# Performance work log

Measured on AMD Instinct MI355X. Metric: run time of the kernel, lower is better.

## Reference

```python
import jax, jax.numpy as jnp
import numpy as np

H, D, G = 8, 32, 32          # heads, dim_head, slice_num
SCALE = D ** -0.5
EPS_LN = 1e-5
EPS_NORM = 1e-5


def layer_norm(x, g, b):
    mu = x.mean(-1, keepdims=True)
    var = x.var(-1, keepdims=True)
    return (x - mu) / jnp.sqrt(var + EPS_LN) * g + b


def setup_inputs() -> dict:
    key = jax.random.key(0)
    ks = jax.random.split(key, 12)
    B, N, C = 4, 32768, 256

    def rn(k, shape, s=0.02):
        return jax.random.normal(k, shape, dtype=jnp.float32) * s

    return {
        "fx": jax.random.normal(ks[0], (B, N, C), dtype=jnp.float32),
        "ln_g": jnp.ones((C,), jnp.float32), "ln_b": jnp.zeros((C,), jnp.float32),
        "Wx": rn(ks[1], (C, H * D)), "bx": jnp.zeros((H * D,), jnp.float32),
        "Wfx": rn(ks[2], (C, H * D)), "bfx": jnp.zeros((H * D,), jnp.float32),
        "Ws": rn(ks[3], (D, G), 0.1), "bs": jnp.zeros((G,), jnp.float32),
        "temp": jnp.full((1, H, 1, 1), 0.5, jnp.float32),
        "Wq": rn(ks[4], (D, D)), "Wk": rn(ks[5], (D, D)), "Wv": rn(ks[6], (D, D)),
        "tln_g": jnp.ones((D,), jnp.float32), "tln_b": jnp.zeros((D,), jnp.float32),
        "W1": rn(ks[7], (D, 4 * D)), "b1": jnp.zeros((4 * D,), jnp.float32),
        "W2": rn(ks[8], (4 * D, D)), "b2": jnp.zeros((D,), jnp.float32),
        "Wo": rn(ks[9], (H * D, C)), "bo": jnp.zeros((C,), jnp.float32),
    }


def reference(fx, ln_g, ln_b, Wx, bx, Wfx, bfx, Ws, bs, temp,
              Wq, Wk, Wv, tln_g, tln_b, W1, b1, W2, b2, Wo, bo):
    B, N, C = fx.shape
    fx_norm = layer_norm(fx, ln_g, ln_b)

    # soft-slice dispatch: project points to per-head features [B,H,N,D]
    x_mid = (fx_norm @ Wx + bx).reshape(B, N, H, D).transpose(0, 2, 1, 3)
    fx_mid = (fx_norm @ Wfx + bfx).reshape(B, N, H, D).transpose(0, 2, 1, 3)
    slice_w = jax.nn.softmax((x_mid @ Ws + bs) / temp, axis=-1)      # [B,H,N,G]
    slice_norm = slice_w.sum(axis=2)                                  # [B,H,G]
    slice_token = jnp.einsum('bhnd,bhng->bhgd', fx_mid, slice_w)
    slice_token = slice_token / (slice_norm + EPS_NORM)[..., None]    # [B,H,G,D]

    # small attention over G=32 slice tokens
    q = slice_token @ Wq
    k = slice_token @ Wk
    v = slice_token @ Wv
    attn = jax.nn.softmax(jnp.einsum('bhgd,bhkd->bhgk', q, k) * SCALE, axis=-1)
    out_tok = jnp.einsum('bhgk,bhkd->bhgd', attn, v) + slice_token

    # token MLP (LN -> Linear -> GELU -> Linear) with residual
    h = layer_norm(out_tok, tln_g, tln_b)
    tokens = (jax.nn.gelu(h @ W1 + b1, approximate=False) @ W2 + b2) + out_tok

    # weighted combine back to points, output projection, residual
    out_x = jnp.einsum('bhgd,bhng->bhnd', tokens, slice_w)
    out_x = out_x.transpose(0, 2, 1, 3).reshape(B, N, H * D)
    return out_x @ Wo + bo + fx_norm
```

## Files before the change

kernel.cpp:

```cpp
#include <hip/hip_runtime.h>
#include <hip/hip_bf16.h>
#include <math.h>

static const int kN = 32768;

typedef __attribute__((ext_vector_type(8))) short short8;
typedef __attribute__((ext_vector_type(4))) float f32x4;

__device__ inline unsigned short f2bf(float x) {
    union { float f; unsigned u; } v; v.f = x;
    unsigned r = v.u + 0x7FFF + ((v.u >> 16) & 1);
    return (unsigned short)(r >> 16);
}

__global__ void k_zero(float* __restrict__ p, int n)
{
    int i = blockIdx.x * 256 + threadIdx.x;
    if (i < n) p[i] = 0.f;
}

__global__ void k_prep(const float* __restrict__ Wx, const float* __restrict__ Ws,
                       const float* __restrict__ bx, const float* __restrict__ bs,
                       const float* __restrict__ Wfx,
                       unsigned short* __restrict__ WxsT, unsigned short* __restrict__ WfxT,
                       float* __restrict__ blog)
{
    __shared__ float ws_s[1024];
    int tid = threadIdx.x;
    for (int i = tid; i < 1024; i += 256) ws_s[i] = Ws[i];
    __syncthreads();
    int c = blockIdx.x;
    int h = tid >> 5, g = tid & 31;
    const float* wrow = &Wx[c * 256 + h * 32];
    float s = 0.f;
    #pragma unroll
    for (int d = 0; d < 32; d++) s += wrow[d] * ws_s[d * 32 + g];
    WxsT[tid * 256 + c] = f2bf(s);
    WfxT[tid * 256 + c] = f2bf(Wfx[c * 256 + tid]);
    if (c == 0) {
        float t = 0.f;
        #pragma unroll
        for (int d = 0; d < 32; d++) t += bx[h * 32 + d] * ws_s[d * 32 + g];
        blog[tid] = t + bs[g];
    }
}

__global__ __launch_bounds__(256) void k_ln(const float* __restrict__ fx,
                                            const float* __restrict__ gam,
                                            const float* __restrict__ bet,
                                            float* __restrict__ out,
                                            unsigned short* __restrict__ outb)
{
    int lane = threadIdx.x & 63;
    long row = (long)blockIdx.x * 4 + (threadIdx.x >> 6);
    float4 v = *(const float4*)&fx[row * 256 + lane * 4];
    float s  = v.x + v.y + v.z + v.w;
    float ss = v.x * v.x + v.y * v.y + v.z * v.z + v.w * v.w;
    for (int off = 32; off; off >>= 1) { s += __shfl_down(s, off); ss += __shfl_down(ss, off); }
    s = __shfl(s, 0); ss = __shfl(ss, 0);
    float mu = s * (1.f / 256.f);
    float rstd = rsqrtf(ss * (1.f / 256.f) - mu * mu + 1e-5f);
    float4 gv = *(const float4*)&gam[lane * 4];
    float4 bv = *(const float4*)&bet[lane * 4];
    float4 o;
    o.x = (v.x - mu) * rstd * gv.x + bv.x;
    o.y = (v.y - mu) * rstd * gv.y + bv.y;
    o.z = (v.z - mu) * rstd * gv.z + bv.z;
    o.w = (v.w - mu) * rstd * gv.w + bv.w;
    *(float4*)&out[row * 256 + lane * 4] = o;
    ushort4 ob;
    ob.x = f2bf(o.x); ob.y = f2bf(o.y); ob.z = f2bf(o.z); ob.w = f2bf(o.w);
    *(ushort4*)&outb[row * 256 + lane * 4] = ob;
}

__global__ __launch_bounds__(256) void k_gemm_mid_mfma(
    const unsigned short* __restrict__ Abf,
    const unsigned short* __restrict__ WxsT, const unsigned short* __restrict__ WfxT,
    const float* __restrict__ blog, const float* __restrict__ bfx,
    const float* __restrict__ temp,
    unsigned short* __restrict__ swb, unsigned short* __restrict__ fmb)
{
    const int mode = blockIdx.y;
    const unsigned short* __restrict__ WT = mode ? WfxT : WxsT;
    const int tid = threadIdx.x;
    const int w = tid >> 6, l = tid & 63;
    const int r16 = l & 15, g4 = l >> 4;
    const long row0 = (long)blockIdx.x * 64;

    __shared__ unsigned short sA[64][40];
    __shared__ unsigned short sB[256][40];

    f32x4 acc[4][4];
    #pragma unroll
    for (int mf = 0; mf < 4; mf++)
        #pragma unroll
        for (int nf = 0; nf < 4; nf++) acc[mf][nf] = (f32x4){0.f, 0.f, 0.f, 0.f};

    const int arow = tid >> 2, apart = tid & 3;
    for (int k0 = 0; k0 < 256; k0 += 32) {
        *(uint4*)&sA[arow][apart * 8] =
            *(const uint4*)&Abf[(row0 + arow) * 256 + k0 + apart * 8];
        #pragma unroll
        for (int p = 0; p < 4; p++) {
            int col = p * 64 + arow;
            *(uint4*)&sB[col][apart * 8] = *(const uint4*)&WT[col * 256 + k0 + apart * 8];
        }
        __syncthreads();
        short8 af[4], bfr[4];
        #pragma unroll
        for (int mf = 0; mf < 4; mf++) af[mf] = *(const short8*)&sA[mf * 16 + r16][g4 * 8];
        #pragma unroll
        for (int nf = 0; nf < 4; nf++) bfr[nf] = *(const short8*)&sB[w * 64 + nf * 16 + r16][g4 * 8];
        #pragma unroll
        for (int mf = 0; mf < 4; mf++)
            #pragma unroll
            for (int nf = 0; nf < 4; nf++)
                acc[mf][nf] = __builtin_amdgcn_mfma_f32_16x16x32_bf16(
                    af[mf], bfr[nf], acc[mf][nf], 0, 0, 0);
        __syncthreads();
    }

    if (mode == 0) {
        float rt0 = 1.0f / temp[w * 2], rt1 = 1.0f / temp[w * 2 + 1];
        float bl00 = blog[w * 64 + r16],      bl01 = blog[w * 64 + 16 + r16];
        float bl10 = blog[w * 64 + 32 + r16], bl11 = blog[w * 64 + 48 + r16];
        #pragma unroll
        for (int mf = 0; mf < 4; mf++) {
            #pragma unroll
            for (int ri = 0; ri < 4; ri++) {
                long row = row0 + mf * 16 + g4 * 4 + ri;
                {
                    float z0 = (acc[mf][0][ri] + bl00) * rt0;
                    float z1 = (acc[mf][1][ri] + bl01) * rt0;
                    float m = fmaxf(z0, z1);
                    m = fmaxf(m, __shfl_xor(m, 1)); m = fmaxf(m, __shfl_xor(m, 2));
                    m = fmaxf(m, __shfl_xor(m, 4)); m = fmaxf(m, __shfl_xor(m, 8));
                    float e0 = __expf(z0 - m), e1 = __expf(z1 - m);
                    float sum = e0 + e1;
                    sum += __shfl_xor(sum, 1); sum += __shfl_xor(sum, 2);
                    sum += __shfl_xor(sum, 4); sum += __shfl_xor(sum, 8);
                    float inv = 1.0f / sum;
                    swb[row * 256 + w * 64 + r16]      = f2bf(e0 * inv);
                    swb[row * 256 + w * 64 + 16 + r16] = f2bf(e1 * inv);
                }
                {
                    float z0 = (acc[mf][2][ri] + bl10) * rt1;
                    float z1 = (acc[mf][3][ri] + bl11) * rt1;
                    float m = fmaxf(z0, z1);
                    m = fmaxf(m, __shfl_xor(m, 1)); m = fmaxf(m, __shfl_xor(m, 2));
                    m = fmaxf(m, __shfl_xor(m, 4)); m = fmaxf(m, __shfl_xor(m, 8));
                    float e0 = __expf(z0 - m), e1 = __expf(z1 - m);
                    float sum = e0 + e1;
                    sum += __shfl_xor(sum, 1); sum += __shfl_xor(sum, 2);
                    sum += __shfl_xor(sum, 4); sum += __shfl_xor(sum, 8);
                    float inv = 1.0f / sum;
                    swb[row * 256 + w * 64 + 32 + r16] = f2bf(e0 * inv);
                    swb[row * 256 + w * 64 + 48 + r16] = f2bf(e1 * inv);
                }
            }
        }
    } else {
        float bb[4];
        #pragma unroll
        for (int nf = 0; nf < 4; nf++) bb[nf] = bfx[w * 64 + nf * 16 + r16];
        #pragma unroll
        for (int mf = 0; mf < 4; mf++)
            #pragma unroll
            for (int nf = 0; nf < 4; nf++)
                #pragma unroll
                for (int ri = 0; ri < 4; ri++) {
                    long row = row0 + mf * 16 + g4 * 4 + ri;
                    fmb[row * 256 + w * 64 + nf * 16 + r16] = f2bf(acc[mf][nf][ri] + bb[nf]);
                }
    }
}

__global__ __launch_bounds__(256) void k_reduce(
    const unsigned short* __restrict__ swb, const unsigned short* __restrict__ fmb,
    float* __restrict__ tok_acc, float* __restrict__ nrm_acc)
{
    const int bh = blockIdx.y;
    const int b = bh >> 3, h = bh & 7;
    const int tid = threadIdx.x;
    const int g = tid >> 3, dq = tid & 7, d0 = dq * 4;
    __shared__ float sw_t[64][36];
    __shared__ float fm_t[64][36];
    float4 acc = make_float4(0.f, 0.f, 0.f, 0.f);
    float nacc = 0.f;
    long base = (long)b * kN + (long)blockIdx.x * 2048;
    const int r = tid >> 2, q = tid & 3;

    for (int t0 = 0; t0 < 2048; t0 += 64) {
        long ga = (base + t0 + r) * 256 + h * 32 + q * 8;
        uint4 wv = *(const uint4*)&swb[ga];
        uint4 fv = *(const uint4*)&fmb[ga];
        __syncthreads();
        const unsigned* wu = (const unsigned*)&wv;
        const unsigned* fu = (const unsigned*)&fv;
        #pragma unroll
        for (int e = 0; e < 4; e++) {
            union { unsigned u; float f; } lo, hi;
            lo.u = wu[e] << 16; hi.u = wu[e] & 0xFFFF0000u;
            sw_t[r][q * 8 + 2 * e] = lo.f; sw_t[r][q * 8 + 2 * e + 1] = hi.f;
            lo.u = fu[e] << 16; hi.u = fu[e] & 0xFFFF0000u;
            fm_t[r][q * 8 + 2 * e] = lo.f; fm_t[r][q * 8 + 2 * e + 1] = hi.f;
        }
        __syncthreads();
        #pragma unroll 4
        for (int rr = 0; rr < 64; rr++) {
            float wgt = sw_t[rr][g];
            float4 f = *(const float4*)&fm_t[rr][d0];
            acc.x += wgt * f.x; acc.y += wgt * f.y; acc.z += wgt * f.z; acc.w += wgt * f.w;
            if (dq == 0) nacc += wgt;
        }
    }
    float* ta = &tok_acc[(bh * 32 + g) * 32 + d0];
    atomicAdd(&ta[0], acc.x); atomicAdd(&ta[1], acc.y);
    atomicAdd(&ta[2], acc.z); atomicAdd(&ta[3], acc.w);
    if (dq == 0) atomicAdd(&nrm_acc[bh * 32 + g], nacc);
}

__global__ __launch_bounds__(256) void k_tokens(
    const float* __restrict__ tok_acc, const float* __restrict__ nrm_acc,
    const float* __restrict__ Wq, const float* __restrict__ Wk, const float* __restrict__ Wv,
    const float* __restrict__ tlng, const float* __restrict__ tlnb,
    const float* __restrict__ W1, const float* __restrict__ b1,
    const float* __restrict__ W2, const float* __restrict__ b2,
    const float* __restrict__ Wo, unsigned short* __restrict__ tokWoT)
{
    const int bh = blockIdx.x, b = bh >> 3, h = bh & 7;
    const int tid = threadIdx.x;
    const int g = tid >> 3, dq = tid & 7, d0 = dq * 4;
    __shared__ float t[32][32], qm[32][32], km[32][32], vm[32][32];
    __shared__ float att[32][33], ot[32][32], hn[32][32], tk[32][32];
    __shared__ float h1[32][128];
    __shared__ float mu_s[32], rs_s[32];

    {
        float inv = 1.0f / (nrm_acc[bh * 32 + g] + 1e-5f);
        #pragma unroll
        for (int u = 0; u < 4; u++)
            t[g][d0 + u] = tok_acc[(bh * 32 + g) * 32 + d0 + u] * inv;
    }
    __syncthreads();
    #pragma unroll
    for (int u = 0; u < 4; u++) {
        int d = d0 + u;
        float sq = 0.f, sk = 0.f, sv = 0.f;
        for (int dd = 0; dd < 32; dd++) {
            float tv = t[g][dd];
            sq = fmaf(tv, Wq[dd * 32 + d], sq);
            sk = fmaf(tv, Wk[dd * 32 + d], sk);
            sv = fmaf(tv, Wv[dd * 32 + d], sv);
        }
        qm[g][d] = sq; km[g][d] = sk; vm[g][d] = sv;
    }
    __syncthreads();
    const float SC = 0.17677669529663687f;
    #pragma unroll
    for (int u = 0; u < 4; u++) {
        int gk = d0 + u;
        float s = 0.f;
        for (int dd = 0; dd < 32; dd++) s = fmaf(qm[g][dd], km[gk][dd], s);
        att[g][gk] = s * SC;
    }
    __syncthreads();
    if (tid < 32) {
        float m = -1e30f;
        for (int j = 0; j < 32; j++) m = fmaxf(m, att[tid][j]);
        float s = 0.f;
        for (int j = 0; j < 32; j++) { float e = expf(att[tid][j] - m); att[tid][j] = e; s += e; }
        float inv = 1.0f / s;
        for (int j = 0; j < 32; j++) att[tid][j] *= inv;
    }
    __syncthreads();
    #pragma unroll
    for (int u = 0; u < 4; u++) {
        int d = d0 + u;
        float s = 0.f;
        for (int kk = 0; kk < 32; kk++) s = fmaf(att[g][kk], vm[kk][d], s);
        ot[g][d] = s + t[g][d];
    }
    __syncthreads();
    if (tid < 32) {
        float s = 0.f, ss = 0.f;
        for (int dd = 0; dd < 32; dd++) { float v = ot[tid][dd]; s += v; ss += v * v; }
        float mu = s * (1.f / 32.f);
        mu_s[tid] = mu;
        rs_s[tid] = rsqrtf(ss * (1.f / 32.f) - mu * mu + 1e-5f);
    }
    __syncthreads();
    #pragma unroll
    for (int u = 0; u < 4; u++) {
        int d = d0 + u;
        hn[g][d] = (ot[g][d] - mu_s[g]) * rs_s[g] * tlng[d] + tlnb[d];
    }
    __syncthreads();
    for (int c = dq * 16; c < dq * 16 + 16; c++) {
        float s = b1[c];
        for (int dd = 0; dd < 32; dd++) s = fmaf(hn[g][dd], W1[dd * 128 + c], s);
        h1[g][c] = 0.5f * s * (1.0f + erff(s * 0.70710678118654752f));
    }
    __syncthreads();
    #pragma unroll
    for (int u = 0; u < 4; u++) {
        int d = d0 + u;
        float s = b2[d];
        for (int c = 0; c < 128; c++) s = fmaf(h1[g][c], W2[c * 32 + d], s);
        tk[g][d] = s + ot[g][d];
    }
    __syncthreads();
    {
        int c0 = dq * 32;
        for (int c = c0; c < c0 + 32; c++) {
            float s = 0.f;
            for (int dd = 0; dd < 32; dd++) s = fmaf(tk[g][dd], Wo[(h * 32 + dd) * 256 + c], s);
            tokWoT[(size_t)b * 65536 + c * 256 + h * 32 + g] = f2bf(s);
        }
    }
}

__global__ __launch_bounds__(256) void k_gemm_out_mfma(
    const unsigned short* __restrict__ Abf,
    const unsigned short* __restrict__ tokWoT,
    const float* __restrict__ bo, const float* __restrict__ fx_norm,
    float* __restrict__ out)
{
    const int tid = threadIdx.x;
    const int w = tid >> 6, l = tid & 63;
    const int r16 = l & 15, g4 = l >> 4;
    const long row0 = (long)blockIdx.x * 64;
    const int b = (int)(row0 >> 15);
    const unsigned short* __restrict__ WT = tokWoT + (size_t)b * 65536;

    __shared__ unsigned short sA[64][40];
    __shared__ unsigned short sB[256][40];

    f32x4 acc[4][4];
    #pragma unroll
    for (int mf = 0; mf < 4; mf++)
        #pragma unroll
        for (int nf = 0; nf < 4; nf++) acc[mf][nf] = (f32x4){0.f, 0.f, 0.f, 0.f};

    const int arow = tid >> 2, apart = tid & 3;
    for (int k0 = 0; k0 < 256; k0 += 32) {
        *(uint4*)&sA[arow][apart * 8] =
            *(const uint4*)&Abf[(row0 + arow) * 256 + k0 + apart * 8];
        #pragma unroll
        for (int p = 0; p < 4; p++) {
            int col = p * 64 + arow;
            *(uint4*)&sB[col][apart * 8] = *(const uint4*)&WT[col * 256 + k0 + apart * 8];
        }
        __syncthreads();
        short8 af[4], bfr[4];
        #pragma unroll
        for (int mf = 0; mf < 4; mf++) af[mf] = *(const short8*)&sA[mf * 16 + r16][g4 * 8];
        #pragma unroll
        for (int nf = 0; nf < 4; nf++) bfr[nf] = *(const short8*)&sB[w * 64 + nf * 16 + r16][g4 * 8];
        #pragma unroll
        for (int mf = 0; mf < 4; mf++)
            #pragma unroll
            for (int nf = 0; nf < 4; nf++)
                acc[mf][nf] = __builtin_amdgcn_mfma_f32_16x16x32_bf16(
                    af[mf], bfr[nf], acc[mf][nf], 0, 0, 0);
        __syncthreads();
    }

    float bb[4];
    #pragma unroll
    for (int nf = 0; nf < 4; nf++) bb[nf] = bo[w * 64 + nf * 16 + r16];
    #pragma unroll
    for (int mf = 0; mf < 4; mf++)
        #pragma unroll
        for (int nf = 0; nf < 4; nf++)
            #pragma unroll
            for (int ri = 0; ri < 4; ri++) {
                long row = row0 + mf * 16 + g4 * 4 + ri;
                int col = w * 64 + nf * 16 + r16;
                out[row * 256 + col] = acc[mf][nf][ri] + bb[nf] + fx_norm[row * 256 + col];
            }
}

extern "C" void kernel_launch(void* const* d_in, const int* in_sizes, int n_in,
                              void* d_out, int out_size, void* d_ws, size_t ws_size,
                              hipStream_t stream)
{
    const float* fx   = (const float*)d_in[0];
    const float* ln_g = (const float*)d_in[1];
    const float* ln_b = (const float*)d_in[2];
    const float* Wx   = (const float*)d_in[3];
    const float* bx   = (const float*)d_in[4];
    const float* Wfx  = (const float*)d_in[5];
    const float* bfx  = (const float*)d_in[6];
    const float* Ws   = (const float*)d_in[7];
    const float* bs   = (const float*)d_in[8];
    const float* temp = (const float*)d_in[9];
    const float* Wq   = (const float*)d_in[10];
    const float* Wk   = (const float*)d_in[11];
    const float* Wv   = (const float*)d_in[12];
    const float* tlng = (const float*)d_in[13];
    const float* tlnb = (const float*)d_in[14];
    const float* W1   = (const float*)d_in[15];
    const float* b1   = (const float*)d_in[16];
    const float* W2   = (const float*)d_in[17];
    const float* b2   = (const float*)d_in[18];
    const float* Wo   = (const float*)d_in[19];
    const float* bo   = (const float*)d_in[20];
    float* out = (float*)d_out;

    char* ws = (char*)d_ws;
    float*          fx_norm = (float*)(ws + 0);
    unsigned short* fxn_bf  = (unsigned short*)(ws + 134217728);
    unsigned short* swb     = (unsigned short*)(ws + 201326592);
    unsigned short* fmb     = (unsigned short*)(ws + 268435456);
    unsigned short* WxsT    = (unsigned short*)(ws + 335544320);
    unsigned short* WfxT    = (unsigned short*)(ws + 335675392);
    float*          blog    = (float*)(ws + 335806464);
    float*          tok_acc = (float*)(ws + 335807488);
    float*          nrm_acc = (float*)(ws + 335938560);
    unsigned short* tokWoT  = (unsigned short*)(ws + 335942656);
    if (ws_size < 336466944ULL) return;

    k_prep<<<256, 256, 0, stream>>>(Wx, Ws, bx, bs, Wfx, WxsT, WfxT, blog);
    k_ln<<<32768, 256, 0, stream>>>(fx, ln_g, ln_b, fx_norm, fxn_bf);
    k_gemm_mid_mfma<<<dim3(2048, 2), 256, 0, stream>>>(fxn_bf, WxsT, WfxT, blog, bfx, temp,
                                                       swb, fmb);
    k_zero<<<132, 256, 0, stream>>>(tok_acc, 33792);
    k_reduce<<<dim3(16, 32), 256, 0, stream>>>(swb, fmb, tok_acc, nrm_acc);
    k_tokens<<<32, 256, 0, stream>>>(tok_acc, nrm_acc, Wq, Wk, Wv, tlng, tlnb,
                                     W1, b1, W2, b2, Wo, tokWoT);
    k_gemm_out_mfma<<<2048, 256, 0, stream>>>(swb, tokWoT, bo, fx_norm, out);
}
```

Baseline: 685.9 us.

## Restructure projection GEMMs with register-resident weights and LDS-staged coalesced stores

Result: slower. 706.8 us (+3.0%).

```diff
diff --git a/kernel.cpp b/kernel.cpp
--- a/kernel.cpp
+++ b/kernel.cpp
@@ -6,6 +6,13 @@
 
 typedef __attribute__((ext_vector_type(8))) short short8;
 typedef __attribute__((ext_vector_type(4))) float f32x4;
+
+typedef __attribute__((address_space(1))) const void* gas_t;
+typedef __attribute__((address_space(3))) void* las_t;
+
+__device__ __forceinline__ void gload16(const void* g, void* l) {
+    __builtin_amdgcn_global_load_lds((gas_t)g, (las_t)l, 16, 0, 0);
+}
 
 __device__ inline unsigned short f2bf(float x) {
     union { float f; unsigned u; } v; v.f = x;
@@ -73,105 +80,135 @@
     *(ushort4*)&outb[row * 256 + lane * 4] = ob;
 }
 
-__global__ __launch_bounds__(256) void k_gemm_mid_mfma(
+__global__ __launch_bounds__(512, 2) void k_gemm_mid_v3(
     const unsigned short* __restrict__ Abf,
     const unsigned short* __restrict__ WxsT, const unsigned short* __restrict__ WfxT,
     const float* __restrict__ blog, const float* __restrict__ bfx,
     const float* __restrict__ temp,
     unsigned short* __restrict__ swb, unsigned short* __restrict__ fmb)
 {
-    const int mode = blockIdx.y;
-    const unsigned short* __restrict__ WT = mode ? WfxT : WxsT;
     const int tid = threadIdx.x;
     const int w = tid >> 6, l = tid & 63;
     const int r16 = l & 15, g4 = l >> 4;
-    const long row0 = (long)blockIdx.x * 64;
-
-    __shared__ unsigned short sA[64][40];
-    __shared__ unsigned short sB[256][40];
-
-    f32x4 acc[4][4];
-    #pragma unroll
-    for (int mf = 0; mf < 4; mf++)
-        #pragma unroll
-        for (int nf = 0; nf < 4; nf++) acc[mf][nf] = (f32x4){0.f, 0.f, 0.f, 0.f};
-
-    const int arow = tid >> 2, apart = tid & 3;
-    for (int k0 = 0; k0 < 256; k0 += 32) {
-        *(uint4*)&sA[arow][apart * 8] =
-            *(const uint4*)&Abf[(row0 + arow) * 256 + k0 + apart * 8];
-        #pragma unroll
-        for (int p = 0; p < 4; p++) {
-            int col = p * 64 + arow;
-            *(uint4*)&sB[col][apart * 8] = *(const uint4*)&WT[col * 256 + k0 + apart * 8];
-        }
-        __syncthreads();
-        short8 af[4], bfr[4];
-        #pragma unroll
-        for (int mf = 0; mf < 4; mf++) af[mf] = *(const short8*)&sA[mf * 16 + r16][g4 * 8];
-        #pragma unroll
-        for (int nf = 0; nf < 4; nf++) bfr[nf] = *(const short8*)&sB[w * 64 + nf * 16 + r16][g4 * 8];
+    const int blk = blockIdx.x;
+
+    __shared__ unsigned short sA[2][64][32];
+    __shared__ unsigned short etile[64][264];
+
+    const unsigned short* WT = (w < 4) ? (WxsT + (size_t)(w * 64) * 256)
+                                       : (WfxT + (size_t)((w - 4) * 64) * 256);
+    short8 bq[4][8];
+    #pragma unroll
+    for (int nf = 0; nf < 4; nf++)
+        #pragma unroll
+        for (int ks = 0; ks < 8; ks++)
+            bq[nf][ks] = *(const short8*)&WT[(size_t)(nf * 16 + r16) * 256 + ks * 32 + g4 * 8];
+
+    float rt0 = 0.f, rt1 = 0.f, bl0 = 0.f, bl1 = 0.f, bl2 = 0.f, bl3 = 0.f;
+    float bf0 = 0.f, bf1 = 0.f, bf2 = 0.f, bf3 = 0.f;
+    if (w < 4) {
+        rt0 = 1.0f / temp[w * 2]; rt1 = 1.0f / temp[w * 2 + 1];
+        bl0 = blog[w * 64 + r16];      bl1 = blog[w * 64 + 16 + r16];
+        bl2 = blog[w * 64 + 32 + r16]; bl3 = blog[w * 64 + 48 + r16];
+    } else {
+        bf0 = bfx[(w - 4) * 64 + r16];      bf1 = bfx[(w - 4) * 64 + 16 + r16];
+        bf2 = bfx[(w - 4) * 64 + 32 + r16]; bf3 = bfx[(w - 4) * 64 + 48 + r16];
+    }
+
+    long row0 = (long)blk * 8 * 64;
+    if (w < 4)
+        gload16(&Abf[(row0 + w * 16 + (l >> 2)) * 256 + (l & 3) * 8], &sA[0][w * 16][0]);
+    __syncthreads();
+
+    for (int j = 0; j < 8; j++) {
+        row0 = (long)(blk * 8 + j) * 64;
+        f32x4 acc[4][4];
         #pragma unroll
         for (int mf = 0; mf < 4; mf++)
             #pragma unroll
-            for (int nf = 0; nf < 4; nf++)
-                acc[mf][nf] = __builtin_amdgcn_mfma_f32_16x16x32_bf16(
-                    af[mf], bfr[nf], acc[mf][nf], 0, 0, 0);
-        __syncthreads();
-    }
-
-    if (mode == 0) {
-        float rt0 = 1.0f / temp[w * 2], rt1 = 1.0f / temp[w * 2 + 1];
-        float bl00 = blog[w * 64 + r16],      bl01 = blog[w * 64 + 16 + r16];
-        float bl10 = blog[w * 64 + 32 + r16], bl11 = blog[w * 64 + 48 + r16];
-        #pragma unroll
-        for (int mf = 0; mf < 4; mf++) {
-            #pragma unroll
-            for (int ri = 0; ri < 4; ri++) {
-                long row = row0 + mf * 16 + g4 * 4 + ri;
-                {
-                    float z0 = (acc[mf][0][ri] + bl00) * rt0;
-                    float z1 = (acc[mf][1][ri] + bl01) * rt0;
-                    float m = fmaxf(z0, z1);
-                    m = fmaxf(m, __shfl_xor(m, 1)); m = fmaxf(m, __shfl_xor(m, 2));
-                    m = fmaxf(m, __shfl_xor(m, 4)); m = fmaxf(m, __shfl_xor(m, 8));
-                    float e0 = __expf(z0 - m), e1 = __expf(z1 - m);
-                    float sum = e0 + e1;
-                    sum += __shfl_xor(sum, 1); sum += __shfl_xor(sum, 2);
-                    sum += __shfl_xor(sum, 4); sum += __shfl_xor(sum, 8);
-                    float inv = 1.0f / sum;
-                    swb[row * 256 + w * 64 + r16]      = f2bf(e0 * inv);
-                    swb[row * 256 + w * 64 + 16 + r16] = f2bf(e1 * inv);
-                }
-                {
-                    float z0 = (acc[mf][2][ri] + bl10) * rt1;
-                    float z1 = (acc[mf][3][ri] + bl11) * rt1;
-                    float m = fmaxf(z0, z1);
-                    m = fmaxf(m, __shfl_xor(m, 1)); m = fmaxf(m, __shfl_xor(m, 2));
-                    m = fmaxf(m, __shfl_xor(m, 4)); m = fmaxf(m, __shfl_xor(m, 8));
-                    float e0 = __expf(z0 - m), e1 = __expf(z1 - m);
-                    float sum = e0 + e1;
-                    sum += __shfl_xor(sum, 1); sum += __shfl_xor(sum, 2);
-                    sum += __shfl_xor(sum, 4); sum += __shfl_xor(sum, 8);
-                    float inv = 1.0f / sum;
-                    swb[row * 256 + w * 64 + 32 + r16] = f2bf(e0 * inv);
-                    swb[row * 256 + w * 64 + 48 + r16] = f2bf(e1 * inv);
+            for (int nf = 0; nf < 4; nf++) acc[mf][nf] = (f32x4){0.f, 0.f, 0.f, 0.f};
+
+        #pragma unroll
+        for (int t = 0; t < 8; t++) {
+            if (w < 4) {
+                if (t < 7)
+                    gload16(&Abf[(row0 + w * 16 + (l >> 2)) * 256 + (t + 1) * 32 + (l & 3) * 8],
+                            &sA[(t + 1) & 1][w * 16][0]);
+                else if (j < 7)
+                    gload16(&Abf[(row0 + 64 + w * 16 + (l >> 2)) * 256 + (l & 3) * 8],
+                            &sA[0][w * 16][0]);
+            }
+            short8 af[4];
+            #pragma unroll
+            for (int mf = 0; mf < 4; mf++)
+                af[mf] = *(const short8*)&sA[t & 1][mf * 16 + r16][g4 * 8];
+            #pragma unroll
+            for (int mf = 0; mf < 4; mf++)
+                #pragma unroll
+                for (int nf = 0; nf < 4; nf++)
+                    acc[mf][nf] = __builtin_amdgcn_mfma_f32_16x16x32_bf16(
+                        af[mf], bq[nf][t], acc[mf][nf], 0, 0, 0);
+            __syncthreads();
+        }
+
+        #pragma unroll
+        for (int half = 0; half < 2; half++) {
+            if ((w >> 2) == half) {
+                if (half == 0) {
+                    #pragma unroll
+                    for (int mf = 0; mf < 4; mf++)
+                        #pragma unroll
+                        for (int ri = 0; ri < 4; ri++) {
+                            int rloc = mf * 16 + g4 * 4 + ri;
+                            float z0 = (acc[mf][0][ri] + bl0) * rt0;
+                            float z1 = (acc[mf][1][ri] + bl1) * rt0;
+                            float m = fmaxf(z0, z1);
+                            m = fmaxf(m, __shfl_xor(m, 1)); m = fmaxf(m, __shfl_xor(m, 2));
+                            m = fmaxf(m, __shfl_xor(m, 4)); m = fmaxf(m, __shfl_xor(m, 8));
+                            float e0 = __expf(z0 - m), e1 = __expf(z1 - m);
+                            float sm = e0 + e1;
+                            sm += __shfl_xor(sm, 1); sm += __shfl_xor(sm, 2);
+                            sm += __shfl_xor(sm, 4); sm += __shfl_xor(sm, 8);
+                            float inv = 1.0f / sm;
+                            etile[rloc][w * 64 + r16]      = f2bf(e0 * inv);
+                            etile[rloc][w * 64 + 16 + r16] = f2bf(e1 * inv);
+                            z0 = (acc[mf][2][ri] + bl2) * rt1;
+                            z1 = (acc[mf][3][ri] + bl3) * rt1;
+                            m = fmaxf(z0, z1);
+                            m = fmaxf(m, __shfl_xor(m, 1)); m = fmaxf(m, __shfl_xor(m, 2));
+                            m = fmaxf(m, __shfl_xor(m, 4)); m = fmaxf(m, __shfl_xor(m, 8));
+                            e0 = __expf(z0 - m); e1 = __expf(z1 - m);
+                            sm = e0 + e1;
+                            sm += __shfl_xor(sm, 1); sm += __shfl_xor(sm, 2);
+                            sm += __shfl_xor(sm, 4); sm += __shfl_xor(sm, 8);
+                            inv = 1.0f / sm;
+                            etile[rloc][w * 64 + 32 + r16] = f2bf(e0 * inv);
+                            etile[rloc][w * 64 + 48 + r16] = f2bf(e1 * inv);
+                        }
+                } else {
+                    int c0 = (w - 4) * 64;
+                    #pragma unroll
+                    for (int mf = 0; mf < 4; mf++)
+                        #pragma unroll
+                        for (int ri = 0; ri < 4; ri++) {
+                            int rloc = mf * 16 + g4 * 4 + ri;
+                            etile[rloc][c0 + r16]      = f2bf(acc[mf][0][ri] + bf0);
+                            etile[rloc][c0 + 16 + r16] = f2bf(acc[mf][1][ri] + bf1);
+                            etile[rloc][c0 + 32 + r16] = f2bf(acc[mf][2][ri] + bf2);
+                            etile[rloc][c0 + 48 + r16] = f2bf(acc[mf][3][ri] + bf3);
+                        }
                 }
             }
-        }
-    } else {
-        float bb[4];
-        #pragma unroll
-        for (int nf = 0; nf < 4; nf++) bb[nf] = bfx[w * 64 + nf * 16 + r16];
-        #pragma unroll
-        for (int mf = 0; mf < 4; mf++)
-            #pragma unroll
-            for (int nf = 0; nf < 4; nf++)
-                #pragma unroll
-                for (int ri = 0; ri < 4; ri++) {
-                    long row = row0 + mf * 16 + g4 * 4 + ri;
-                    fmb[row * 256 + w * 64 + nf * 16 + r16] = f2bf(acc[mf][nf][ri] + bb[nf]);
-                }
+            __syncthreads();
+            unsigned short* dst = half ? fmb : swb;
+            #pragma unroll
+            for (int k = 0; k < 4; k++) {
+                int c = tid + 512 * k;
+                int row = c >> 5, col = (c & 31) * 8;
+                *(uint4*)&dst[(row0 + row) * 256 + col] = *(const uint4*)&etile[row][col];
+            }
+            __syncthreads();
+        }
     }
 }
 
@@ -320,7 +357,7 @@
     }
 }
 
-__global__ __launch_bounds__(256) void k_gemm_out_mfma(
+__global__ __launch_bounds__(512, 2) void k_gemm_out_v3(
     const unsigned short* __restrict__ Abf,
     const unsigned short* __restrict__ tokWoT,
     const float* __restrict__ bo, const float* __restrict__ fx_norm,
@@ -329,56 +366,84 @@
     const int tid = threadIdx.x;
     const int w = tid >> 6, l = tid & 63;
     const int r16 = l & 15, g4 = l >> 4;
-    const long row0 = (long)blockIdx.x * 64;
-    const int b = (int)(row0 >> 15);
-    const unsigned short* __restrict__ WT = tokWoT + (size_t)b * 65536;
-
-    __shared__ unsigned short sA[64][40];
-    __shared__ unsigned short sB[256][40];
-
-    f32x4 acc[4][4];
-    #pragma unroll
-    for (int mf = 0; mf < 4; mf++)
-        #pragma unroll
-        for (int nf = 0; nf < 4; nf++) acc[mf][nf] = (f32x4){0.f, 0.f, 0.f, 0.f};
-
-    const int arow = tid >> 2, apart = tid & 3;
-    for (int k0 = 0; k0 < 256; k0 += 32) {
-        *(uint4*)&sA[arow][apart * 8] =
-            *(const uint4*)&Abf[(row0 + arow) * 256 + k0 + apart * 8];
-        #pragma unroll
-        for (int p = 0; p < 4; p++) {
-            int col = p * 64 + arow;
-            *(uint4*)&sB[col][apart * 8] = *(const uint4*)&WT[col * 256 + k0 + apart * 8];
-        }
-        __syncthreads();
-        short8 af[4], bfr[4];
-        #pragma unroll
-        for (int mf = 0; mf < 4; mf++) af[mf] = *(const short8*)&sA[mf * 16 + r16][g4 * 8];
-        #pragma unroll
-        for (int nf = 0; nf < 4; nf++) bfr[nf] = *(const short8*)&sB[w * 64 + nf * 16 + r16][g4 * 8];
+    const int blk = blockIdx.x;
+    const int wc = w & 3, wrh = w >> 2;
+    const int b = blk >> 6;
+
+    __shared__ unsigned short sA[2][128][32];
+    __shared__ float etf[64][260];
+
+    const unsigned short* WT = tokWoT + (size_t)b * 65536 + (size_t)(wc * 64) * 256;
+    short8 bq[4][8];
+    #pragma unroll
+    for (int nf = 0; nf < 4; nf++)
+        #pragma unroll
+        for (int ks = 0; ks < 8; ks++)
+            bq[nf][ks] = *(const short8*)&WT[(size_t)(nf * 16 + r16) * 256 + ks * 32 + g4 * 8];
+
+    long row0 = (long)blk * 4 * 128;
+    gload16(&Abf[(row0 + w * 16 + (l >> 2)) * 256 + (l & 3) * 8], &sA[0][w * 16][0]);
+    __syncthreads();
+
+    for (int j = 0; j < 4; j++) {
+        row0 = (long)(blk * 4 + j) * 128;
+        f32x4 acc[4][4];
         #pragma unroll
         for (int mf = 0; mf < 4; mf++)
             #pragma unroll
-            for (int nf = 0; nf < 4; nf++)
-                acc[mf][nf] = __builtin_amdgcn_mfma_f32_16x16x32_bf16(
-                    af[mf], bfr[nf], acc[mf][nf], 0, 0, 0);
-        __syncthreads();
-    }
-
-    float bb[4];
-    #pragma unroll
-    for (int nf = 0; nf < 4; nf++) bb[nf] = bo[w * 64 + nf * 16 + r16];
-    #pragma unroll
-    for (int mf = 0; mf < 4; mf++)
-        #pragma unroll
-        for (int nf = 0; nf < 4; nf++)
-            #pragma unroll
-            for (int ri = 0; ri < 4; ri++) {
-                long row = row0 + mf * 16 + g4 * 4 + ri;
-                int col = w * 64 + nf * 16 + r16;
-                out[row * 256 + col] = acc[mf][nf][ri] + bb[nf] + fx_norm[row * 256 + col];
+            for (int nf = 0; nf < 4; nf++) acc[mf][nf] = (f32x4){0.f, 0.f, 0.f, 0.f};
+
+        #pragma unroll
+        for (int t = 0; t < 8; t++) {
+            if (t < 7)
+                gload16(&Abf[(row0 + w * 16 + (l >> 2)) * 256 + (t + 1) * 32 + (l & 3) * 8],
+                        &sA[(t + 1) & 1][w * 16][0]);
+            else if (j < 3)
+                gload16(&Abf[(row0 + 128 + w * 16 + (l >> 2)) * 256 + (l & 3) * 8],
+                        &sA[0][w * 16][0]);
+            short8 af[4];
+            #pragma unroll
+            for (int mf = 0; mf < 4; mf++)
+                af[mf] = *(const short8*)&sA[t & 1][wrh * 64 + mf * 16 + r16][g4 * 8];
+            #pragma unroll
+            for (int mf = 0; mf < 4; mf++)
+                #pragma unroll
+                for (int nf = 0; nf < 4; nf++)
+                    acc[mf][nf] = __builtin_amdgcn_mfma_f32_16x16x32_bf16(
+                        af[mf], bq[nf][t], acc[mf][nf], 0, 0, 0);
+            __syncthreads();
+        }
+
+        #pragma unroll
+        for (int half = 0; half < 2; half++) {
+            if (wrh == half) {
+                #pragma unroll
+                for (int mf = 0; mf < 4; mf++)
+                    #pragma unroll
+                    for (int nf = 0; nf < 4; nf++)
+                        #pragma unroll
+                        for (int ri = 0; ri < 4; ri++)
+                            etf[mf * 16 + g4 * 4 + ri][wc * 64 + nf * 16 + r16] = acc[mf][nf][ri];
             }
+            __syncthreads();
+            #pragma unroll
+            for (int k = 0; k < 8; k++) {
+                int c = tid + 512 * k;
+                int row = c >> 6, col = (c & 63) * 4;
+                float4 v = *(const float4*)&etf[row][col];
+                float4 bb = *(const float4*)&bo[col];
+                long gr = row0 + half * 64 + row;
+                float4 fn = *(const float4*)&fx_norm[gr * 256 + col];
+                float4 o;
+                o.x = v.x + bb.x + fn.x;
+                o.y = v.y + bb.y + fn.y;
+                o.z = v.z + bb.z + fn.z;
+                o.w = v.w + bb.w + fn.w;
+                *(float4*)&out[gr * 256 + col] = o;
+            }
+            __syncthreads();
+        }
+    }
 }
 
 extern "C" void kernel_launch(void* const* d_in, const int* in_sizes, int n_in,
@@ -423,11 +488,10 @@
 
     k_prep<<<256, 256, 0, stream>>>(Wx, Ws, bx, bs, Wfx, WxsT, WfxT, blog);
     k_ln<<<32768, 256, 0, stream>>>(fx, ln_g, ln_b, fx_norm, fxn_bf);
-    k_gemm_mid_mfma<<<dim3(2048, 2), 256, 0, stream>>>(fxn_bf, WxsT, WfxT, blog, bfx, temp,
-                                                       swb, fmb);
+    k_gemm_mid_v3<<<256, 512, 0, stream>>>(fxn_bf, WxsT, WfxT, blog, bfx, temp, swb, fmb);
     k_zero<<<132, 256, 0, stream>>>(tok_acc, 33792);
     k_reduce<<<dim3(16, 32), 256, 0, stream>>>(swb, fmb, tok_acc, nrm_acc);
     k_tokens<<<32, 256, 0, stream>>>(tok_acc, nrm_acc, Wq, Wk, Wv, tlng, tlnb,
                                      W1, b1, W2, b2, Wo, tokWoT);
-    k_gemm_out_mfma<<<2048, 256, 0, stream>>>(swb, tokWoT, bo, fx_norm, out);
-}
+    k_gemm_out_v3<<<256, 512, 0, stream>>>(swb, tokWoT, bo, fx_norm, out);
+}
```
